# Kernel optimization log

Hardware: AMD Instinct MI355X
Metric: run time of the kernel (lower is better)

The kernel has to match this reference:

```python
import jax, jax.numpy as jnp
import numpy as np

N_PARENT = 50000   # parent voxels
C_IN = 256
C_OUT = 256
FANOUT = 8         # children per parent (kernel 2, stride 2 generative conv)
N_TGT = 200000     # number of ground-truth-occupied child indices


def setup_inputs() -> dict:
    key = jax.random.key(0)
    k_fea, k_wup, k_wcls, k_idx = jax.random.split(key, 4)
    fea = jax.random.normal(k_fea, (N_PARENT, C_IN), dtype=jnp.float32)
    W_up = jax.random.normal(k_wup, (FANOUT, C_IN, C_OUT), dtype=jnp.float32) * (1.0 / np.sqrt(C_IN))
    b_up = jnp.zeros((C_OUT,), dtype=jnp.float32)
    W_cls = jax.random.normal(k_wcls, (C_OUT, 1), dtype=jnp.float32) * (1.0 / np.sqrt(C_OUT))
    b_cls = jnp.zeros((1,), dtype=jnp.float32)
    # kernel_map in-indices into the upsampled coordinate set (GT-occupied children)
    target_idx = jax.random.randint(k_idx, (N_TGT,), 0, N_PARENT * FANOUT, dtype=jnp.int64)
    return {"fea": fea, "W_up": W_up, "b_up": b_up, "W_cls": W_cls,
            "b_cls": b_cls, "target_idx": target_idx}


def reference(fea, W_up, b_up, W_cls, b_cls, target_idx):
    # upsample_block: generative transposed sparse conv. Every parent voxel emits
    # FANOUT children, each via its own [C_IN, C_OUT] kernel slice.
    # [N, C_IN] x [K, C_IN, C_OUT] -> [N, K, C_OUT] -> [N*K, C_OUT]
    fea_up = jnp.einsum('nc,kcd->nkd', fea, W_up).reshape(-1, W_up.shape[2]) + b_up
    # classify_block: 1-channel existence logit
    exist = fea_up @ W_cls + b_cls                      # [N*K, 1]
    # keep = exist > 0 (computed under no_grad in torch)
    keep = jax.lax.stop_gradient(exist[:, 0]) > 0       # [N*K] bool
    # kernel_map target scatter: target[curr_in] = 1
    n_up = fea_up.shape[0]
    target = jnp.zeros((n_up,), dtype=jnp.bool_).at[target_idx].set(True)
    keep = keep | target                                # training: keep |= target
    # MinkowskiPruning(fea, keep): jit-compatible masking instead of compaction
    fea_pruned = jnp.where(keep[:, None], fea_up, jnp.zeros((), fea_up.dtype))
    return fea_pruned, exist, target
```

## Files before the change

### kernel.cpp

```cpp
#include <hip/hip_runtime.h>
#include <hip/hip_bf16.h>

#define N_PARENT 50000
#define C_IN     256
#define C_OUT    256
#define FANOUT   8
#define N_TGT    200000
#define N_UP     (N_PARENT * FANOUT)
#define NCOL     (FANOUT * C_OUT)
#define NSTRIP   391
#define NROWS    (NSTRIP * 128)

#define OFF_A    0u
#define OFF_B    (NSTRIP * 65536u)
#define OFF_V    (OFF_B + 16u * 65536u)
#define OFF_EB   (OFF_V + 8192u)
#define OFF_KEEP (OFF_EB + 256u)

typedef __attribute__((ext_vector_type(8))) short short8;
typedef __attribute__((ext_vector_type(4))) float floatx4;

static __device__ __forceinline__ unsigned short f2bf(float f) {
    return __builtin_bit_cast(unsigned short, __float2bfloat16(f));
}

static __device__ __forceinline__ void gload_lds16(const void* gsrc, void* ldsdst) {
    __builtin_amdgcn_global_load_lds(
        (const __attribute__((address_space(1))) unsigned int*)gsrc,
        (__attribute__((address_space(3))) unsigned int*)ldsdst, 16, 0, 0);
}

__global__ __launch_bounds__(256) void prep_kernel(
        const float* __restrict__ W_up, const float* __restrict__ b_up,
        const float* __restrict__ W_cls, const float* __restrict__ b_cls,
        unsigned char* __restrict__ ws, float* __restrict__ out2) {
    __shared__ float sm[4];
    const int bid = blockIdx.x;
    const int k = bid >> 8, c = bid & 255;
    const int d = threadIdx.x;

    if (d < 49) {
        const int i4 = bid * 49 + d;
        if (i4 < N_UP / 4)
            *(floatx4*)&out2[i4 * 4] = (floatx4){0.f, 0.f, 0.f, 0.f};
    }

    const float w = W_up[((k * 256 + c) * 256) + d];
    const int bn = (k << 1) | (d >> 7);
    const int jr = d & 127;
    const int t  = c >> 5;
    const int ch = (c >> 3) & 3;
    const int e  = c & 7;
    const unsigned off = OFF_B + (unsigned)bn * 65536u + (unsigned)t * 8192u
                       + (unsigned)jr * 64u + (unsigned)((ch ^ (jr & 3)) << 4)
                       + (unsigned)(e << 1);
    *(unsigned short*)(ws + off) = f2bf(w);

    float p = w * W_cls[d];
    #pragma unroll
    for (int m = 1; m < 64; m <<= 1) p += __shfl_xor(p, m);
    if ((d & 63) == 0) sm[d >> 6] = p;
    __syncthreads();
    if (d == 0)
        ((float*)(ws + OFF_V))[k * 256 + c] = sm[0] + sm[1] + sm[2] + sm[3];

    if (bid == 0) {
        __syncthreads();
        float q = b_up[d] * W_cls[d];
        #pragma unroll
        for (int m = 1; m < 64; m <<= 1) q += __shfl_xor(q, m);
        if ((d & 63) == 0) sm[d >> 6] = q;
        __syncthreads();
        if (d == 0)
            *((float*)(ws + OFF_EB)) = sm[0] + sm[1] + sm[2] + sm[3] + b_cls[0];
    }
}

__global__ __launch_bounds__(256) void scatter_kernel(
        const int* __restrict__ idx, float* __restrict__ out2) {
    int i = blockIdx.x * 256 + threadIdx.x;
    if (i < N_TGT) out2[idx[i]] = 1.0f;
}

__global__ __launch_bounds__(256) void convert_kernel(
        const float* __restrict__ fea, const float* __restrict__ target,
        float* __restrict__ out1, unsigned char* __restrict__ ws) {
    const float* V = (const float*)(ws + OFF_V);
    const float eb = *(const float*)(ws + OFF_EB);

    const int rowid = blockIdx.x * 4 + (threadIdx.x >> 6);
    const int lane  = threadIdx.x & 63;
    const bool valid = rowid < N_PARENT;

    floatx4 f = (floatx4){0.f, 0.f, 0.f, 0.f};
    if (valid)
        f = __builtin_nontemporal_load(
                (const floatx4*)&fea[(size_t)rowid * C_IN + lane * 4]);

    float ex[8];
    #pragma unroll
    for (int k = 0; k < 8; ++k) {
        const float4 v = *(const float4*)&V[k * 256 + lane * 4];
        ex[k] = f[0] * v.x + f[1] * v.y + f[2] * v.z + f[3] * v.w;
    }

    const unsigned long long pk =
          (unsigned long long)f2bf(f[0])
        | ((unsigned long long)f2bf(f[1]) << 16)
        | ((unsigned long long)f2bf(f[2]) << 32)
        | ((unsigned long long)f2bf(f[3]) << 48);
    const int strip = rowid >> 7, r = rowid & 127;
    const int t = lane >> 3, ch = (lane >> 1) & 3, half = lane & 1;
    const unsigned off = OFF_A + (unsigned)strip * 65536u + (unsigned)t * 8192u
                       + (unsigned)r * 64u + (unsigned)((ch ^ (r & 3)) << 4)
                       + (unsigned)(half * 8);
    *(unsigned long long*)(ws + off) = pk;

    #pragma unroll
    for (int m = 8; m < 64; m <<= 1)
        #pragma unroll
        for (int k = 0; k < 8; ++k) ex[k] += __shfl_xor(ex[k], m);

    const int ksel = lane >> 3;
    float v = ex[0];
    #pragma unroll
    for (int k = 1; k < 8; ++k) v = (ksel == k) ? ex[k] : v;
    #pragma unroll
    for (int m = 1; m < 8; m <<= 1) v += __shfl_xor(v, m);
    v += eb;

    if ((lane & 7) == 0 && valid) {
        const size_t o = (size_t)rowid * FANOUT + ksel;
        out1[o] = v;
        ws[OFF_KEEP + o] = ((v > 0.0f) || (target[o] != 0.0f)) ? 1 : 0;
    }
}

__global__ __launch_bounds__(256, 4) void gemm_kernel(
        const float* __restrict__ b_up, const unsigned char* __restrict__ ws,
        float* __restrict__ out0) {
    __shared__ unsigned short As[2][4096];
    __shared__ unsigned short Bs[2][4096];
    __shared__ unsigned char keeps[128];

    const int bid = blockIdx.x;
    const int g = bid & 7, u = bid >> 3;
    const int tt = u >> 4, bn = u & 15;
    const int bm = g + 8 * tt;
    if (bm >= NSTRIP) return;

    const unsigned char* Abase = ws + OFF_A + (size_t)bm * 65536u;
    const unsigned char* Bbase = ws + OFF_B + (size_t)bn * 65536u;

    const int tid  = threadIdx.x;
    const int lane = tid & 63;
    const int wid  = tid >> 6;
    const int wr = wid >> 1, wc = wid & 1;
    const int llo = lane & 15, lhi = lane >> 4;

    if (tid < 128) {
        const int n = bm * 128 + tid;
        keeps[tid] = (n < N_PARENT) ? ws[OFF_KEEP + (size_t)n * FANOUT + (bn >> 1)] : 0;
    }

    floatx4 acc[4][4];
    #pragma unroll
    for (int a = 0; a < 4; ++a)
        #pragma unroll
        for (int b = 0; b < 4; ++b) acc[a][b] = (floatx4){0.f, 0.f, 0.f, 0.f};

    gload_lds16(Abase + tid * 16,        (char*)As[0] + tid * 16);
    gload_lds16(Abase + 4096 + tid * 16, (char*)As[0] + 4096 + tid * 16);
    gload_lds16(Bbase + tid * 16,        (char*)Bs[0] + tid * 16);
    gload_lds16(Bbase + 4096 + tid * 16, (char*)Bs[0] + 4096 + tid * 16);
    __syncthreads();

    #pragma unroll
    for (int t = 0; t < 8; ++t) {
        const int cur = t & 1;
        if (t < 7) {
            const unsigned o = (unsigned)(t + 1) * 8192u;
            gload_lds16(Abase + o + tid * 16,        (char*)As[cur ^ 1] + tid * 16);
            gload_lds16(Abase + o + 4096 + tid * 16, (char*)As[cur ^ 1] + 4096 + tid * 16);
            gload_lds16(Bbase + o + tid * 16,        (char*)Bs[cur ^ 1] + tid * 16);
            gload_lds16(Bbase + o + 4096 + tid * 16, (char*)Bs[cur ^ 1] + 4096 + tid * 16);
        }

        short8 af[4], bf[4];
        #pragma unroll
        for (int fm = 0; fm < 4; ++fm) {
            const int row = wr * 64 + fm * 16 + llo;
            const int ch = lhi ^ (row & 3);
            af[fm] = *(const short8*)((const char*)As[cur] + row * 64 + ch * 16);
        }
        #pragma unroll
        for (int fn = 0; fn < 4; ++fn) {
            const int row = wc * 64 + fn * 16 + llo;
            const int ch = lhi ^ (row & 3);
            bf[fn] = *(const short8*)((const char*)Bs[cur] + row * 64 + ch * 16);
        }
        #pragma unroll
        for (int fm = 0; fm < 4; ++fm)
            #pragma unroll
            for (int fn = 0; fn < 4; ++fn)
                acc[fm][fn] = __builtin_amdgcn_mfma_f32_16x16x32_bf16(
                    bf[fn], af[fm], acc[fm][fn], 0, 0, 0);

        if (t < 7) __syncthreads();
    }

    const int j0 = bn * 128;
    #pragma unroll
    for (int fm = 0; fm < 4; ++fm) {
        const int row = wr * 64 + fm * 16 + llo;
        const int m = bm * 128 + row;
        if (m >= N_PARENT) continue;
        const bool kp = keeps[row] != 0;
        #pragma unroll
        for (int fn = 0; fn < 4; ++fn) {
            const int j = j0 + wc * 64 + fn * 16 + lhi * 4;
            const float4 bv = *(const float4*)&b_up[j & 255];
            const floatx4 a = acc[fm][fn];
            floatx4 o;
            o[0] = kp ? a[0] + bv.x : 0.0f;
            o[1] = kp ? a[1] + bv.y : 0.0f;
            o[2] = kp ? a[2] + bv.z : 0.0f;
            o[3] = kp ? a[3] + bv.w : 0.0f;
            __builtin_nontemporal_store(o, (floatx4*)&out0[(size_t)m * NCOL + j]);
        }
    }
}

extern "C" void kernel_launch(void* const* d_in, const int* in_sizes, int n_in,
                              void* d_out, int out_size, void* d_ws, size_t ws_size,
                              hipStream_t stream) {
    const float* fea   = (const float*)d_in[0];
    const float* W_up  = (const float*)d_in[1];
    const float* b_up  = (const float*)d_in[2];
    const float* W_cls = (const float*)d_in[3];
    const float* b_cls = (const float*)d_in[4];
    const int*   tidx  = (const int*)d_in[5];

    float* out0 = (float*)d_out;
    float* out1 = out0 + (size_t)N_UP * C_OUT;
    float* out2 = out1 + N_UP;
    unsigned char* ws = (unsigned char*)d_ws;

    prep_kernel<<<2048, 256, 0, stream>>>(W_up, b_up, W_cls, b_cls, ws, out2);
    scatter_kernel<<<(N_TGT + 255) / 256, 256, 0, stream>>>(tidx, out2);
    convert_kernel<<<NROWS / 4, 256, 0, stream>>>(fea, out2, out1, ws);
    gemm_kernel<<<392 * 16, 256, 0, stream>>>(b_up, ws, out0);
}
```

Measured before the change: 151.1 us.

## Restructure GEMM K-loop into two-stage prefetch with explicit vmcnt waits

Replaces the double-buffered K loop, which issued the next tile's loads and then used __syncthreads, with a schedule that prefetches two tiles ahead. Each iteration waits on vmcnt for the current tile and issues a barrier. It reads the fragments into registers, then barriers again and reuses the same buffer for tile t+2 while the MFMAs run. This is meant to hide more global-to-LDS latency behind compute and to drop the full waitcnt that __syncthreads implies. In exchange there are two barriers per iteration, and correctness depends on the hand-tuned vmcnt counts matching the compiler's load ordering.

```diff
diff --git a/kernel.cpp b/kernel.cpp
--- a/kernel.cpp
+++ b/kernel.cpp
@@ -29,6 +29,9 @@
         (const __attribute__((address_space(1))) unsigned int*)gsrc,
         (__attribute__((address_space(3))) unsigned int*)ldsdst, 16, 0, 0);
 }
+
+#define SCHED_BAR() __builtin_amdgcn_sched_barrier(0)
+#define SBAR()      __builtin_amdgcn_s_barrier()
 
 __global__ __launch_bounds__(256) void prep_kernel(
         const float* __restrict__ W_up, const float* __restrict__ b_up,
@@ -169,22 +172,24 @@
         #pragma unroll
         for (int b = 0; b < 4; ++b) acc[a][b] = (floatx4){0.f, 0.f, 0.f, 0.f};
 
-    gload_lds16(Abase + tid * 16,        (char*)As[0] + tid * 16);
-    gload_lds16(Abase + 4096 + tid * 16, (char*)As[0] + 4096 + tid * 16);
-    gload_lds16(Bbase + tid * 16,        (char*)Bs[0] + tid * 16);
-    gload_lds16(Bbase + 4096 + tid * 16, (char*)Bs[0] + 4096 + tid * 16);
-    __syncthreads();
+    #pragma unroll
+    for (int t0 = 0; t0 < 2; ++t0) {
+        const unsigned o = (unsigned)t0 * 8192u;
+        gload_lds16(Abase + o + tid * 16,        (char*)As[t0] + tid * 16);
+        gload_lds16(Abase + o + 4096 + tid * 16, (char*)As[t0] + 4096 + tid * 16);
+        gload_lds16(Bbase + o + tid * 16,        (char*)Bs[t0] + tid * 16);
+        gload_lds16(Bbase + o + 4096 + tid * 16, (char*)Bs[t0] + 4096 + tid * 16);
+    }
 
     #pragma unroll
     for (int t = 0; t < 8; ++t) {
         const int cur = t & 1;
-        if (t < 7) {
-            const unsigned o = (unsigned)(t + 1) * 8192u;
-            gload_lds16(Abase + o + tid * 16,        (char*)As[cur ^ 1] + tid * 16);
-            gload_lds16(Abase + o + 4096 + tid * 16, (char*)As[cur ^ 1] + 4096 + tid * 16);
-            gload_lds16(Bbase + o + tid * 16,        (char*)Bs[cur ^ 1] + tid * 16);
-            gload_lds16(Bbase + o + 4096 + tid * 16, (char*)Bs[cur ^ 1] + 4096 + tid * 16);
-        }
+
+        if (t < 7) asm volatile("s_waitcnt vmcnt(4)" ::: "memory");
+        else       asm volatile("s_waitcnt vmcnt(0)" ::: "memory");
+        SCHED_BAR();
+        SBAR();
+        SCHED_BAR();
 
         short8 af[4], bf[4];
         #pragma unroll
@@ -199,14 +204,26 @@
             const int ch = lhi ^ (row & 3);
             bf[fn] = *(const short8*)((const char*)Bs[cur] + row * 64 + ch * 16);
         }
+
+        asm volatile("s_waitcnt lgkmcnt(0)" ::: "memory");
+        SCHED_BAR();
+        SBAR();
+        SCHED_BAR();
+
+        if (t < 6) {
+            const unsigned o = (unsigned)(t + 2) * 8192u;
+            gload_lds16(Abase + o + tid * 16,        (char*)As[cur] + tid * 16);
+            gload_lds16(Abase + o + 4096 + tid * 16, (char*)As[cur] + 4096 + tid * 16);
+            gload_lds16(Bbase + o + tid * 16,        (char*)Bs[cur] + tid * 16);
+            gload_lds16(Bbase + o + 4096 + tid * 16, (char*)Bs[cur] + 4096 + tid * 16);
+        }
+
         #pragma unroll
         for (int fm = 0; fm < 4; ++fm)
             #pragma unroll
             for (int fn = 0; fn < 4; ++fn)
                 acc[fm][fn] = __builtin_amdgcn_mfma_f32_16x16x32_bf16(
                     bf[fn], af[fm], acc[fm][fn], 0, 0, 0);
-
-        if (t < 7) __syncthreads();
     }
 
     const int j0 = bn * 128;
```

Measured after the change: 148.8 us, median of 2. About the same (-1.5%).

## Load GEMM fragments directly from global memory, dropping LDS staging

Applied to the files above, without the earlier changes.

The GEMM kernel no longer stages A/B tiles through double-buffered LDS with global_load_lds and barriers. Each lane now reads its bf16 MFMA fragments straight from the pre-packed workspace, so the XOR swizzle in the prep kernels is removed. Keep flags are also read per lane from global memory rather than through shared memory. This removes LDS traffic, barriers and the LDS occupancy limit (launch bounds relaxed), but loses cross-wave reuse: each tile is fetched from L2/global by both waves sharing it, and there is no explicit prefetch to hide latency.

```diff
diff --git a/kernel.cpp b/kernel.cpp
--- a/kernel.cpp
+++ b/kernel.cpp
@@ -24,12 +24,6 @@
     return __builtin_bit_cast(unsigned short, __float2bfloat16(f));
 }
 
-static __device__ __forceinline__ void gload_lds16(const void* gsrc, void* ldsdst) {
-    __builtin_amdgcn_global_load_lds(
-        (const __attribute__((address_space(1))) unsigned int*)gsrc,
-        (__attribute__((address_space(3))) unsigned int*)ldsdst, 16, 0, 0);
-}
-
 __global__ __launch_bounds__(256) void prep_kernel(
         const float* __restrict__ W_up, const float* __restrict__ b_up,
         const float* __restrict__ W_cls, const float* __restrict__ b_cls,
@@ -49,10 +43,10 @@
     const int bn = (k << 1) | (d >> 7);
     const int jr = d & 127;
     const int t  = c >> 5;
-    const int ch = (c >> 3) & 3;
+    const int g  = (c >> 3) & 3;
     const int e  = c & 7;
     const unsigned off = OFF_B + (unsigned)bn * 65536u + (unsigned)t * 8192u
-                       + (unsigned)jr * 64u + (unsigned)((ch ^ (jr & 3)) << 4)
+                       + (unsigned)jr * 64u + (unsigned)(g << 4)
                        + (unsigned)(e << 1);
     *(unsigned short*)(ws + off) = f2bf(w);
 
@@ -110,9 +104,9 @@
         | ((unsigned long long)f2bf(f[2]) << 32)
         | ((unsigned long long)f2bf(f[3]) << 48);
     const int strip = rowid >> 7, r = rowid & 127;
-    const int t = lane >> 3, ch = (lane >> 1) & 3, half = lane & 1;
+    const int t = lane >> 3, g = (lane >> 1) & 3, half = lane & 1;
     const unsigned off = OFF_A + (unsigned)strip * 65536u + (unsigned)t * 8192u
-                       + (unsigned)r * 64u + (unsigned)((ch ^ (r & 3)) << 4)
+                       + (unsigned)r * 64u + (unsigned)(g << 4)
                        + (unsigned)(half * 8);
     *(unsigned long long*)(ws + off) = pk;
 
@@ -136,32 +130,25 @@
     }
 }
 
-__global__ __launch_bounds__(256, 4) void gemm_kernel(
+__global__ __launch_bounds__(256) void gemm_kernel(
         const float* __restrict__ b_up, const unsigned char* __restrict__ ws,
         float* __restrict__ out0) {
-    __shared__ unsigned short As[2][4096];
-    __shared__ unsigned short Bs[2][4096];
-    __shared__ unsigned char keeps[128];
-
     const int bid = blockIdx.x;
     const int g = bid & 7, u = bid >> 3;
     const int tt = u >> 4, bn = u & 15;
     const int bm = g + 8 * tt;
     if (bm >= NSTRIP) return;
 
-    const unsigned char* Abase = ws + OFF_A + (size_t)bm * 65536u;
-    const unsigned char* Bbase = ws + OFF_B + (size_t)bn * 65536u;
-
     const int tid  = threadIdx.x;
     const int lane = tid & 63;
     const int wid  = tid >> 6;
     const int wr = wid >> 1, wc = wid & 1;
     const int llo = lane & 15, lhi = lane >> 4;
 
-    if (tid < 128) {
-        const int n = bm * 128 + tid;
-        keeps[tid] = (n < N_PARENT) ? ws[OFF_KEEP + (size_t)n * FANOUT + (bn >> 1)] : 0;
-    }
+    const unsigned char* Aw = ws + OFF_A + (size_t)bm * 65536u
+                            + (unsigned)((wr * 64 + llo) * 64 + lhi * 16);
+    const unsigned char* Bw = ws + OFF_B + (size_t)bn * 65536u
+                            + (unsigned)((wc * 64 + llo) * 64 + lhi * 16);
 
     floatx4 acc[4][4];
     #pragma unroll
@@ -169,63 +156,47 @@
         #pragma unroll
         for (int b = 0; b < 4; ++b) acc[a][b] = (floatx4){0.f, 0.f, 0.f, 0.f};
 
-    gload_lds16(Abase + tid * 16,        (char*)As[0] + tid * 16);
-    gload_lds16(Abase + 4096 + tid * 16, (char*)As[0] + 4096 + tid * 16);
-    gload_lds16(Bbase + tid * 16,        (char*)Bs[0] + tid * 16);
-    gload_lds16(Bbase + 4096 + tid * 16, (char*)Bs[0] + 4096 + tid * 16);
-    __syncthreads();
-
     #pragma unroll
     for (int t = 0; t < 8; ++t) {
-        const int cur = t & 1;
-        if (t < 7) {
-            const unsigned o = (unsigned)(t + 1) * 8192u;
-            gload_lds16(Abase + o + tid * 16,        (char*)As[cur ^ 1] + tid * 16);
-            gload_lds16(Abase + o + 4096 + tid * 16, (char*)As[cur ^ 1] + 4096 + tid * 16);
-            gload_lds16(Bbase + o + tid * 16,        (char*)Bs[cur ^ 1] + tid * 16);
-            gload_lds16(Bbase + o + 4096 + tid * 16, (char*)Bs[cur ^ 1] + 4096 + tid * 16);
-        }
-
         short8 af[4], bf[4];
         #pragma unroll
-        for (int fm = 0; fm < 4; ++fm) {
-            const int row = wr * 64 + fm * 16 + llo;
-            const int ch = lhi ^ (row & 3);
-            af[fm] = *(const short8*)((const char*)As[cur] + row * 64 + ch * 16);
-        }
-        #pragma unroll
-        for (int fn = 0; fn < 4; ++fn) {
-            const int row = wc * 64 + fn * 16 + llo;
-            const int ch = lhi ^ (row & 3);
-            bf[fn] = *(const short8*)((const char*)Bs[cur] + row * 64 + ch * 16);
-        }
+        for (int fm = 0; fm < 4; ++fm)
+            af[fm] = *(const short8*)(Aw + t * 8192 + fm * 1024);
+        #pragma unroll
+        for (int fn = 0; fn < 4; ++fn)
+            bf[fn] = *(const short8*)(Bw + t * 8192 + fn * 1024);
         #pragma unroll
         for (int fm = 0; fm < 4; ++fm)
             #pragma unroll
             for (int fn = 0; fn < 4; ++fn)
                 acc[fm][fn] = __builtin_amdgcn_mfma_f32_16x16x32_bf16(
                     bf[fn], af[fm], acc[fm][fn], 0, 0, 0);
-
-        if (t < 7) __syncthreads();
+    }
+
+    const int kk = bn >> 1;
+    bool kp[4];
+    #pragma unroll
+    for (int fm = 0; fm < 4; ++fm) {
+        const int m = bm * 128 + wr * 64 + fm * 16 + llo;
+        kp[fm] = (m < N_PARENT) &&
+                 (ws[OFF_KEEP + (size_t)m * FANOUT + kk] != 0);
     }
 
     const int j0 = bn * 128;
     #pragma unroll
     for (int fm = 0; fm < 4; ++fm) {
-        const int row = wr * 64 + fm * 16 + llo;
-        const int m = bm * 128 + row;
+        const int m = bm * 128 + wr * 64 + fm * 16 + llo;
         if (m >= N_PARENT) continue;
-        const bool kp = keeps[row] != 0;
         #pragma unroll
         for (int fn = 0; fn < 4; ++fn) {
             const int j = j0 + wc * 64 + fn * 16 + lhi * 4;
             const float4 bv = *(const float4*)&b_up[j & 255];
             const floatx4 a = acc[fm][fn];
             floatx4 o;
-            o[0] = kp ? a[0] + bv.x : 0.0f;
-            o[1] = kp ? a[1] + bv.y : 0.0f;
-            o[2] = kp ? a[2] + bv.z : 0.0f;
-            o[3] = kp ? a[3] + bv.w : 0.0f;
+            o[0] = kp[fm] ? a[0] + bv.x : 0.0f;
+            o[1] = kp[fm] ? a[1] + bv.y : 0.0f;
+            o[2] = kp[fm] ? a[2] + bv.z : 0.0f;
+            o[3] = kp[fm] ? a[3] + bv.w : 0.0f;
             __builtin_nontemporal_store(o, (floatx4*)&out0[(size_t)m * NCOL + j]);
         }
     }
```

Result: slower. 196.9 us (+30.3%).
